# Performance work log

Hardware: AMD Instinct MI355X
Metric: run time of the kernel (lower is better)

Reference implementation:

```python
import jax, jax.numpy as jnp
import numpy as np

# Constants derived from init_kwargs / input shapes
B = 4          # number of graphs (equal-sized point clouds)
N = 16384      # points per graph
STRIDE = 4     # center_sampler: strided sampling, ratio 0.25 -> M = N/4
K = 20         # k nearest neighbors
N_SCAL = 16    # reps '16x0+16x1': 16 scalars
N_VEC = 16     # 16 vectors (3 coeffs each)
D = N_SCAL + 3 * N_VEC   # 64 feature coeffs
HID = 128
OUT = 128


def transform_coeffs(x, R):
    """TensorReps('16x0+16x1') coefficient transform: scalars unchanged,
    each 3-vector v -> R @ v.  x: [n, D], R: [n, 3, 3]."""
    s = x[:, :N_SCAL]
    v = x[:, N_SCAL:].reshape(-1, N_VEC, 3)
    v = jnp.einsum('nab,nkb->nka', R, v)
    return jnp.concatenate([s, v.reshape(-1, 3 * N_VEC)], axis=-1)


def setup_inputs() -> dict:
    key = jax.random.key(0)
    ks = jax.random.split(key, 6)
    Ntot = B * N
    x = jax.random.normal(ks[0], (Ntot, D), jnp.float32)
    pos = jax.random.normal(ks[1], (Ntot, 3), jnp.float32)
    # orthonormal local frames via QR of random 3x3 matrices
    lf = jax.random.normal(ks[2], (Ntot, 3, 3), jnp.float32)
    lframes, _ = jnp.linalg.qr(lf)
    batch = jnp.repeat(jnp.arange(B, dtype=jnp.int32), N)
    W1 = jax.random.normal(ks[3], (2 * D, HID), jnp.float32) / np.sqrt(2 * D)
    b1 = jnp.zeros((HID,), jnp.float32)
    W2 = jax.random.normal(ks[4], (HID, OUT), jnp.float32) / np.sqrt(HID)
    b2 = jnp.zeros((OUT,), jnp.float32)
    return {"x": x, "pos": pos, "lframes": lframes, "batch": batch,
            "W1": W1, "b1": b1, "W2": W2, "b2": b2}


def reference(x, pos, lframes, batch, W1, b1, W2, b2):
    M = N // STRIDE
    # --- center_sampler: strided sampling per graph (CustomPointSampler) ---
    idx = (jnp.arange(B)[:, None] * N + jnp.arange(0, N, STRIDE)[None, :]).reshape(-1)  # [B*M]

    # --- transform features to global frame: coeffs with lframes^T ---
    kf = transform_coeffs(x, jnp.swapaxes(lframes, -1, -2))
    # --- concat_pos_to_features (transform_pos=False) ---
    kf = jnp.concatenate([kf, pos], axis=-1)            # [Ntot, 67]
    Dk = kf.shape[-1]

    # --- brute-force per-graph kNN: centers query against all nodes ---
    kf_b = kf.reshape(B, N, Dk)
    q = kf_b[:, ::STRIDE]                               # [B, M, Dk] centers
    d2 = (jnp.sum(q * q, -1)[:, :, None]
          + jnp.sum(kf_b * kf_b, -1)[:, None, :]
          - 2.0 * jnp.einsum('bmd,bnd->bmn', q, kf_b))  # [B, M, N]
    _, nbr = jax.lax.top_k(-d2, K)                      # [B, M, K] per-graph idx
    src = nbr + (jnp.arange(B) * N)[:, None, None]      # global node idx

    # --- gather dst/src node data ---
    x_dst = x[idx].reshape(B, M, D)
    lf_dst = lframes[idx]                               # [B*M, 3, 3]
    x_src = x[src.reshape(-1)].reshape(B, M, K, D)

    # --- EdgeConv (tensor-frames flavor): relative features rotated into the
    #     destination local frame, MLP over [x_i, R_i (x_j - x_i)], max-aggr ---
    rel = x_src - x_dst[:, :, None]                     # [B, M, K, D]
    R_edge = jnp.repeat(lf_dst, K, axis=0)              # [B*M*K, 3, 3]
    rel_local = transform_coeffs(rel.reshape(-1, D), R_edge).reshape(B, M, K, D)
    h = jnp.concatenate(
        [jnp.broadcast_to(x_dst[:, :, None], rel.shape), rel_local], axis=-1)  # [B,M,K,2D]
    msg = jax.nn.relu(h @ W1 + b1) @ W2 + b2            # [B, M, K, OUT]
    out = jnp.max(msg, axis=2).reshape(B * M, OUT)

    return out, pos[idx], batch[idx], lf_dst
```

## Files before the change

kernel.cpp:

```cpp
#include <hip/hip_runtime.h>
#include <hip/hip_bf16.h>

#define NTOT 65536
#define KNN  20
#define KROW 104

typedef __attribute__((ext_vector_type(4))) float f32x4;
typedef __attribute__((ext_vector_type(8))) short s16x8;

#define WS_NORM 13631488
#define WS_NBR  13893632
#define WS_WT1  15204352
#define WS_WT2  15237120
#define WS_MG   15269888

#define ROWS 144
#define CSTR 257
#define OFF_TAUG 149056
#define KNN_SMEM 149312
#define THRESH 64

__device__ __forceinline__ unsigned short f2bf_rne(float v){
  unsigned u = __float_as_uint(v);
  return (unsigned short)((u + 0x7FFFu + ((u >> 16) & 1u)) >> 16);
}

__global__ __launch_bounds__(256) void k_prep(const float* __restrict__ x,
        const float* __restrict__ pos, const float* __restrict__ lfr,
        unsigned short* __restrict__ kfB, float* __restrict__ normB){
  int n = blockIdx.x * 256 + threadIdx.x;
  const float* xr = x + n * 64;
  float R[9];
  #pragma unroll
  for (int j = 0; j < 9; j++) R[j] = lfr[n * 9 + j];
  float c[67];
  #pragma unroll
  for (int i = 0; i < 16; i++) c[i] = xr[i];
  #pragma unroll
  for (int k = 0; k < 16; k++){
    float v0 = xr[16 + 3*k], v1 = xr[17 + 3*k], v2 = xr[18 + 3*k];
    #pragma unroll
    for (int a = 0; a < 3; a++)
      c[16 + 3*k + a] = R[a] * v0 + R[3 + a] * v1 + R[6 + a] * v2;
  }
  #pragma unroll
  for (int a = 0; a < 3; a++) c[64 + a] = pos[n * 3 + a];
  float sq = 0.f;
  #pragma unroll
  for (int d = 0; d < 67; d++) sq += c[d] * c[d];
  __attribute__((aligned(16))) unsigned short row[KROW];
  #pragma unroll
  for (int d = 0; d < 67; d++) row[d] = f2bf_rne(c[d]);
  #pragma unroll
  for (int d = 67; d < KROW; d++) row[d] = 0;
  uint4* dst = (uint4*)(kfB + (size_t)n * KROW);
  const uint4* s4 = (const uint4*)row;
  #pragma unroll
  for (int i = 0; i < 13; i++) dst[i] = s4[i];
  normB[n] = sq;
}

__global__ __launch_bounds__(256) void k_wprep(const float* __restrict__ W1,
        const float* __restrict__ W2, unsigned short* __restrict__ wb1,
        unsigned short* __restrict__ wb2){
  int a = blockIdx.x * 256 + threadIdx.x;
  int kb = a >> 12, n = (a >> 5) & 127, kl = a & 31;
  int i = ((kb << 5) + kl) * 128 + n;
  wb1[a] = f2bf_rne(W1[i]);
  wb2[a] = f2bf_rne(W2[i]);
}

__device__ __forceinline__ unsigned col_compact(unsigned* buf,
    int col, int cn, int lane){
  unsigned e0 = (lane < cn) ? buf[lane * CSTR + col] : 0xFFFFFFFFu;
  unsigned e1 = (lane + 64 < cn) ? buf[(lane + 64) * CSTR + col] : 0xFFFFFFFFu;
  unsigned T = 0;
  #pragma unroll 1
  for (int b = 31; b >= 0; --b){
    unsigned cand = T | (1u << b);
    int c = __popcll(__ballot(e0 < cand)) + __popcll(__ballot(e1 < cand));
    if (c <= 31) T = cand;
  }
  unsigned long long m0 = __ballot(e0 <= T);
  unsigned long long m1 = __ballot(e1 <= T);
  int b1 = __popcll(m0);
  unsigned long long ltm = (1ull << lane) - 1ull;
  if (e0 <= T) buf[__popcll(m0 & ltm) * CSTR + col] = e0;
  if (e1 <= T) buf[(b1 + __popcll(m1 & ltm)) * CSTR + col] = e1;
  return T;
}

__global__ __launch_bounds__(1024, 4) void k_knn(
    const unsigned short* __restrict__ kfB, const float* __restrict__ normB,
    unsigned short* __restrict__ mgG){
  __shared__ __attribute__((aligned(16))) char smem[KNN_SMEM];
  unsigned* buf = (unsigned*)smem;
  unsigned* tauG = (unsigned*)(smem + OFF_TAUG);

  int tid = threadIdx.x;
  int blk = blockIdx.x;
  int b = blk & 3;
  int qloc0 = (blk >> 2) << 6;
  int bbase = b << 14;

  if (tid < 64) tauG[tid] = 0x7F7FC000u;

  int lane = tid & 63;
  int wv = tid >> 6;
  int wq = wv >> 2;
  int kq = wv & 3;
  int l15 = lane & 15, quad = lane >> 4;
  int colB = (wq << 6) + kq;

  int qloc = qloc0 + (wq << 4);
  s16x8 af[3];
  {
    int nodeA = bbase + ((qloc + l15) << 2);
    const unsigned short* ap = kfB + (size_t)nodeA * KROW + quad * 8;
    af[0] = *(const s16x8*)(ap);
    af[1] = *(const s16x8*)(ap + 32);
    af[2] = *(const s16x8*)(ap + 64);
  }
  float qsq[4];
  #pragma unroll
  for (int r = 0; r < 4; r++)
    qsq[r] = normB[bbase + ((qloc + (quad << 2) + r) << 2)];

  float tauR[4] = {3.0e38f, 3.0e38f, 3.0e38f, 3.0e38f};
  int cntR[4];

  const unsigned short* kp = kfB + (size_t)(bbase + (kq << 12) + l15) * KROW + quad * 8;
  const float* np = normB + (bbase + (kq << 12) + l15);

  __syncthreads();

  s16x8 cK[4][3];
  float nK[4];
  #define LOADK(S) do { \
      cK[S][0] = *(const s16x8*)(kp); \
      cK[S][1] = *(const s16x8*)(kp + 32); \
      cK[S][2] = *(const s16x8*)(kp + 64); \
      nK[S] = *np; kp += 16 * KROW; np += 16; } while (0)

  auto comp = [&](const s16x8 bf[3], float ksqv, float d2v[4]){
    f32x4 acc = (f32x4){0.f, 0.f, 0.f, 0.f};
    acc = __builtin_amdgcn_mfma_f32_16x16x32_bf16(af[0], bf[0], acc, 0, 0, 0);
    acc = __builtin_amdgcn_mfma_f32_16x16x32_bf16(af[1], bf[1], acc, 0, 0, 0);
    acc = __builtin_amdgcn_mfma_f32_16x16x32_bf16(af[2], bf[2], acc, 0, 0, 0);
    #pragma unroll
    for (int r = 0; r < 4; r++)
      d2v[r] = fmaxf(qsq[r] + ksqv - 2.f * acc[r], 0.f);
  };

  auto seed = [&](const float d2v[4], int g){
    int kidx = (kq << 12) + (g << 4) + l15;
    #pragma unroll
    for (int r = 0; r < 4; r++){
      unsigned pk = ((__float_as_uint(d2v[r]) + 0x2000u) & 0xFFFFC000u) | (unsigned)kidx;
      buf[((g << 4) + l15) * CSTR + colB + (quad << 4) + (r << 2)] = pk;
    }
  };

  auto process = [&](const float d2v[4], int g){
    bool p[4];
    #pragma unroll
    for (int r = 0; r < 4; r++) p[r] = d2v[r] < tauR[r];
    if (__any(p[0] | p[1] | p[2] | p[3])){
      int kidx = (kq << 12) + (g << 4) + l15;
      #pragma unroll
      for (int r = 0; r < 4; r++){
        unsigned long long m = __ballot(p[r]);
        if (m){
          int lo = (int)((m >> (quad << 4)) & 0xFFFFull);
          if (lo){
            int colr = colB + (quad << 4) + (r << 2);
            int pre = __popc(lo & ((1 << l15) - 1));
            if (p[r]){
              unsigned pk = ((__float_as_uint(d2v[r]) + 0x2000u) & 0xFFFFC000u) | (unsigned)kidx;
              buf[(cntR[r] + pre) * CSTR + colr] = pk;
            }
            cntR[r] += __popc(lo);
          }
        }
      }
    }
  };

  auto check_compact = [&](int limit){
    #pragma unroll
    for (int r = 0; r < 4; r++){
      unsigned long long mr = __ballot(cntR[r] > limit);
      while (mr){
        int ldr = __ffsll((unsigned long long)mr) - 1;
        int qd = ldr >> 4;
        mr &= ~(0xFFFFull << (qd << 4));
        int col = colB + (qd << 4) + (r << 2);
        int cn = __shfl(cntR[r], qd << 4, 64);
        unsigned T = col_compact(buf, col, cn, lane);
        if (quad == qd) cntR[r] = 32;
        if (lane == 0) atomicMin(&tauG[(wq << 4) + (qd << 2) + r], T);
      }
    }
  };

  float d2v[4];
  LOADK(0); LOADK(1); LOADK(2); LOADK(3);
  #pragma unroll
  for (int j = 0; j < 4; j++){
    comp(cK[j], nK[j], d2v);
    seed(d2v, j);
    LOADK(j);
  }
  #pragma unroll
  for (int r = 0; r < 4; r++) cntR[r] = 64;

  #pragma unroll 1
  for (int g = 4; g < 256; g += 4){
    #pragma unroll
    for (int j = 0; j < 4; j++){
      comp(cK[j], nK[j], d2v);
      LOADK(j);
      process(d2v, g + j);
    }
    check_compact(THRESH);
    uint4 tg = *(const uint4*)&tauG[(wq << 4) + (quad << 2)];
    tauR[0] = __uint_as_float(tg.x & 0xFFFFC000u);
    tauR[1] = __uint_as_float(tg.y & 0xFFFFC000u);
    tauR[2] = __uint_as_float(tg.z & 0xFFFFC000u);
    tauR[3] = __uint_as_float(tg.w & 0xFFFFC000u);
  }

  check_compact(32);
  __syncthreads();

  #pragma unroll 1
  for (int s = 0; s < 4; s++){
    int q = (wv << 2) + s;
    int qid = (b << 12) + qloc0 + q;
    unsigned e0 = buf[(lane & 31) * CSTR + (q << 2) + (lane >> 5)];
    unsigned e1 = buf[(lane & 31) * CSTR + (q << 2) + 2 + (lane >> 5)];
    unsigned T = 0;
    #pragma unroll 1
    for (int bb = 31; bb >= 0; --bb){
      unsigned cand = T | (1u << bb);
      int c = __popcll(__ballot(e0 < cand)) + __popcll(__ballot(e1 < cand));
      if (c <= 31) T = cand;
    }
    unsigned long long m0 = __ballot(e0 <= T);
    unsigned long long m1 = __ballot(e1 <= T);
    int b1 = __popcll(m0);
    unsigned long long ltm = (1ull << lane) - 1ull;
    int p0 = __popcll(m0 & ltm);
    int p1 = b1 + __popcll(m1 & ltm);
    if ((e0 <= T) && (p0 < 32)) mgG[qid * 32 + p0] = (unsigned short)(e0 & 0x3FFFu);
    if ((e1 <= T) && (p1 < 32)) mgG[qid * 32 + p1] = (unsigned short)(e1 & 0x3FFFu);
  }
}

__global__ __launch_bounds__(256) void k_rerank(const float* __restrict__ x,
    const float* __restrict__ pos, const float* __restrict__ lfr,
    const unsigned short* __restrict__ mgG, int* __restrict__ nbr){
  __shared__ double qkf[8][68];
  int tid = threadIdx.x;
  int ql = tid >> 5;
  int j  = tid & 31;
  int qid = blockIdx.x * 8 + ql;
  int b = qid >> 12;
  int bbase = b << 14;
  int node_q = bbase + ((qid & 4095) << 2);

  {
    const float* xr = x + node_q * 64;
    for (int dd = j; dd < 67; dd += 32){
      double val;
      if (dd < 16) val = (double)xr[dd];
      else if (dd < 64){
        int r = dd - 16; int k = r / 3; int a = r - 3 * k;
        val = (double)lfr[node_q*9 + a]     * (double)xr[16 + 3*k]
            + (double)lfr[node_q*9 + 3 + a] * (double)xr[17 + 3*k]
            + (double)lfr[node_q*9 + 6 + a] * (double)xr[18 + 3*k];
      } else val = (double)pos[node_q*3 + (dd - 64)];
      qkf[ql][dd] = val;
    }
  }
  __syncthreads();

  int idx = (int)mgG[qid * 32 + j];
  int node = bbase + idx;
  const float* xr = x + node * 64;
  double R[9];
  #pragma unroll
  for (int t = 0; t < 9; t++) R[t] = (double)lfr[node * 9 + t];
  double d2 = 0.0;
  #pragma unroll
  for (int dd = 0; dd < 16; dd++){ double t = (double)xr[dd] - qkf[ql][dd]; d2 += t * t; }
  #pragma unroll
  for (int k = 0; k < 16; k++){
    double v0 = xr[16 + 3*k], v1 = xr[17 + 3*k], v2 = xr[18 + 3*k];
    #pragma unroll
    for (int a = 0; a < 3; a++){
      double val = R[a] * v0 + R[3 + a] * v1 + R[6 + a] * v2;
      double t = val - qkf[ql][16 + 3*k + a]; d2 += t * t;
    }
  }
  #pragma unroll
  for (int a = 0; a < 3; a++){ double t = (double)pos[node*3 + a] - qkf[ql][64 + a]; d2 += t * t; }

  int base = (tid & 32) ? 32 : 0;
  int rank = 0;
  #pragma unroll 1
  for (int j2 = 0; j2 < 32; j2++){
    double o = __shfl(d2, base + j2, 64);
    rank += (o < d2) || ((o == d2) && (j2 < j));
  }
  if (rank < KNN) nbr[qid * KNN + rank] = node;
}

#define M_X   0
#define M_H   43520
#define M_W1  84480
#define M_W2  117248
#define M_B1  150016
#define M_B2  150528
#define M_NBR 151040
#define M_XD  151680
#define M_LF  153728
#define M_SZ  154048

__global__ __launch_bounds__(512) void k_mlp(const float* __restrict__ x,
    const float* __restrict__ lfr, const int* __restrict__ nbr,
    const unsigned short* __restrict__ wb1, const unsigned short* __restrict__ wb2,
    const float* __restrict__ b1, const float* __restrict__ b2,
    float* __restrict__ out){
  __shared__ __attribute__((aligned(16))) char smem[M_SZ];
  float* xsF = (float*)(smem + M_X);
  unsigned short* a1B = (unsigned short*)(smem + M_X);
  unsigned short* hB = (unsigned short*)(smem + M_H);
  unsigned short* wt1 = (unsigned short*)(smem + M_W1);
  unsigned short* wt2 = (unsigned short*)(smem + M_W2);
  float* b1L = (float*)(smem + M_B1);
  float* b2L = (float*)(smem + M_B2);
  int*   nbrL = (int*)(smem + M_NBR);
  float* xdL  = (float*)(smem + M_XD);
  float* lfL  = (float*)(smem + M_LF);

  int tid = threadIdx.x;
  int qid0 = blockIdx.x * 8;
  int lane = tid & 63, wv = tid >> 6;
  int l15 = lane & 15, quad = lane >> 4;

  {
    const uint4* g1 = (const uint4*)wb1;
    const uint4* g2 = (const uint4*)wb2;
    uint4* l1 = (uint4*)wt1;
    uint4* l2 = (uint4*)wt2;
    #pragma unroll
    for (int p = 0; p < 4; p++){
      l1[tid + (p << 9)] = g1[tid + (p << 9)];
      l2[tid + (p << 9)] = g2[tid + (p << 9)];
    }
  }
  if (tid < 160) nbrL[tid] = nbr[qid0 * 20 + tid];
  {
    int q = tid >> 6, d = tid & 63;
    int qid = qid0 + q;
    int node = ((qid >> 12) << 14) + ((qid & 4095) << 2);
    xdL[q * 64 + d] = x[node * 64 + d];
  }
  if (tid < 72){
    int q = tid / 9, j = tid - 9 * q;
    int qid = qid0 + q;
    int node = ((qid >> 12) << 14) + ((qid & 4095) << 2);
    lfL[q * 9 + j] = lfr[node * 9 + j];
  }
  if (tid < 128){ b1L[tid] = b1[tid]; b2L[tid] = b2[tid]; }
  __syncthreads();

  {
    int f4 = tid & 15;
    #pragma unroll
    for (int p = 0; p < 5; p++){
      int e = (tid >> 4) + (p << 5);
      float4 v = *(const float4*)&x[(size_t)nbrL[e] * 64 + (f4 << 2)];
      *(float4*)&xsF[e * 68 + (f4 << 2)] = v;
    }
  }
  __syncthreads();

  {
    int d = tid & 127, eo = tid >> 7;
    int cls, kk = 0, aa = 0;
    if (d < 64) cls = 0;
    else { int dd = d - 64;
      if (dd < 16) cls = 1;
      else { cls = 2; int r = dd - 16; kk = (r * 21846) >> 16; aa = r - 3 * kk; } }
    int hoff = ((d >> 5) * 160) * 32 + (d & 31);
    #pragma unroll 4
    for (int p = 0; p < 40; p++){
      int e = eo + (p << 2);
      int q = (e * 3277) >> 16;
      float v;
      if (cls == 0) v = xdL[q * 64 + d];
      else if (cls == 1) v = xsF[e * 68 + (d - 64)] - xdL[q * 64 + (d - 64)];
      else {
        int base = 16 + 3 * kk;
        float u0 = xsF[e * 68 + base]     - xdL[q * 64 + base];
        float u1 = xsF[e * 68 + base + 1] - xdL[q * 64 + base + 1];
        float u2 = xsF[e * 68 + base + 2] - xdL[q * 64 + base + 2];
        v = lfL[q * 9 + aa * 3] * u0 + lfL[q * 9 + aa * 3 + 1] * u1 + lfL[q * 9 + aa * 3 + 2] * u2;
      }
      hB[hoff + e * 32] = f2bf_rne(v);
    }
  }
  __syncthreads();

  {
    s16x8 bfr[4];
    #pragma unroll
    for (int ks = 0; ks < 4; ks++)
      bfr[ks] = *(const s16x8*)(wt1 + ((ks * 128 + (wv << 4) + l15) * 32 + (quad << 3)));
    float b1v = b1L[(wv << 4) + l15];
    int colhi = wv >> 1, collo = ((wv & 1) << 4) + l15;
    #pragma unroll
    for (int mt = 0; mt < 10; mt++){
      f32x4 acc = (f32x4){0.f, 0.f, 0.f, 0.f};
      #pragma unroll
      for (int ks = 0; ks < 4; ks++){
        s16x8 af = *(const s16x8*)(hB + ((ks * 160 + (mt << 4) + l15) * 32 + (quad << 3)));
        acc = __builtin_amdgcn_mfma_f32_16x16x32_bf16(af, bfr[ks], acc, 0, 0, 0);
      }
      #pragma unroll
      for (int r = 0; r < 4; r++){
        float v = fmaxf(acc[r] + b1v, 0.f);
        int row = (mt << 4) + (quad << 2) + r;
        a1B[(colhi * 160 + row) * 32 + collo] = f2bf_rne(v);
      }
    }
  }
  __syncthreads();

  {
    s16x8 bfr[4];
    #pragma unroll
    for (int ks = 0; ks < 4; ks++)
      bfr[ks] = *(const s16x8*)(wt2 + ((ks * 128 + (wv << 4) + l15) * 32 + (quad << 3)));
    float mxv[8];
    #pragma unroll
    for (int q = 0; q < 8; q++) mxv[q] = -3.0e38f;
    const int QA[10]  = {0,0,1,2,3,4,4,5,6,7};
    const int CUT[10] = {16,4,8,12,16,16,4,8,12,16};
    #pragma unroll
    for (int mt = 0; mt < 10; mt++){
      f32x4 acc = (f32x4){0.f, 0.f, 0.f, 0.f};
      #pragma unroll
      for (int ks = 0; ks < 4; ks++){
        s16x8 af = *(const s16x8*)(a1B + ((ks * 160 + (mt << 4) + l15) * 32 + (quad << 3)));
        acc = __builtin_amdgcn_mfma_f32_16x16x32_bf16(af, bfr[ks], acc, 0, 0, 0);
      }
      int qa = QA[mt], cut = CUT[mt];
      if (cut >= 16){
        #pragma unroll
        for (int r = 0; r < 4; r++) mxv[qa] = fmaxf(mxv[qa], acc[r]);
      } else {
        #pragma unroll
        for (int r = 0; r < 4; r++){
          int lr = (quad << 2) + r;
          bool toA = lr < cut;
          mxv[qa]     = fmaxf(mxv[qa],     toA ? acc[r] : -3.0e38f);
          mxv[qa + 1] = fmaxf(mxv[qa + 1], toA ? -3.0e38f : acc[r]);
        }
      }
    }
    #pragma unroll
    for (int q = 0; q < 8; q++){
      float v = mxv[q];
      v = fmaxf(v, __shfl_xor(v, 16, 64));
      v = fmaxf(v, __shfl_xor(v, 32, 64));
      mxv[q] = v;
    }
    if (quad == 0){
      int col = (wv << 4) + l15;
      float b2v = b2L[col];
      #pragma unroll
      for (int q = 0; q < 8; q++)
        out[(size_t)(qid0 + q) * 128 + col] = mxv[q] + b2v;
    }
  }
}

__global__ __launch_bounds__(256) void k_tail(const float* __restrict__ pos,
    const float* __restrict__ lfr, float* __restrict__ out){
  int q = blockIdx.x * 256 + threadIdx.x;
  int b = q >> 12;
  int node = (b << 14) + ((q & 4095) << 2);
  float* o_pos = out + 2097152;
  float* o_bat = out + 2146304;
  float* o_lf  = out + 2162688;
  #pragma unroll
  for (int j = 0; j < 3; j++) o_pos[q * 3 + j] = pos[node * 3 + j];
  o_bat[q] = (float)b;
  #pragma unroll
  for (int j = 0; j < 9; j++) o_lf[q * 9 + j] = lfr[node * 9 + j];
}

extern "C" void kernel_launch(void* const* d_in, const int* in_sizes, int n_in,
                              void* d_out, int out_size, void* d_ws, size_t ws_size,
                              hipStream_t stream){
  const float* x   = (const float*)d_in[0];
  const float* pos = (const float*)d_in[1];
  const float* lfr = (const float*)d_in[2];
  const float* W1  = (const float*)d_in[4];
  const float* b1  = (const float*)d_in[5];
  const float* W2  = (const float*)d_in[6];
  const float* b2  = (const float*)d_in[7];

  unsigned short* kfB = (unsigned short*)d_ws;
  float* normB = (float*)((char*)d_ws + WS_NORM);
  int*   nbr   = (int*)((char*)d_ws + WS_NBR);
  unsigned short* wb1 = (unsigned short*)((char*)d_ws + WS_WT1);
  unsigned short* wb2 = (unsigned short*)((char*)d_ws + WS_WT2);
  unsigned short* mgG = (unsigned short*)((char*)d_ws + WS_MG);
  float* out = (float*)d_out;

  hipLaunchKernelGGL(k_prep,   dim3(256),  dim3(256),  0, stream, x, pos, lfr, kfB, normB);
  hipLaunchKernelGGL(k_wprep,  dim3(64),   dim3(256),  0, stream, W1, W2, wb1, wb2);
  hipLaunchKernelGGL(k_knn,    dim3(256),  dim3(1024), 0, stream, kfB, normB, mgG);
  hipLaunchKernelGGL(k_rerank, dim3(2048), dim3(256),  0, stream, x, pos, lfr, mgG, nbr);
  hipLaunchKernelGGL(k_mlp,    dim3(2048), dim3(512),  0, stream, x, lfr, nbr, wb1, wb2, b1, b2, out);
  hipLaunchKernelGGL(k_tail,   dim3(64),   dim3(256),  0, stream, pos, lfr, out);
}
```

Measured before the change: 597.4 us.

## Coarsen kNN compaction threshold bits and load MLP weights directly to registers

The in-loop candidate compaction now searches only the upper 18 bits of the key, keeping every candidate at or below the coarse threshold and returning that count, which cuts ballot iterations per compaction. The exact 32-entry compaction runs only in the final pass. The MLP kernel no longer stages W1/W2 in shared memory; each wave loads its weight fragments straight from global memory into registers, shrinking LDS use so more blocks can be resident per CU. The risks are more candidates kept after each coarse compaction, which can trigger compactions more often, and extra register pressure from the weight fragments.

Result: faster. 535.6 us (-10.3%).

```diff
diff --git a/kernel.cpp b/kernel.cpp
--- a/kernel.cpp
+++ b/kernel.cpp
@@ -70,7 +70,7 @@
   wb2[a] = f2bf_rne(W2[i]);
 }
 
-__device__ __forceinline__ unsigned col_compact(unsigned* buf,
+__device__ __forceinline__ unsigned col_compact32(unsigned* buf,
     int col, int cn, int lane){
   unsigned e0 = (lane < cn) ? buf[lane * CSTR + col] : 0xFFFFFFFFu;
   unsigned e1 = (lane + 64 < cn) ? buf[(lane + 64) * CSTR + col] : 0xFFFFFFFFu;
@@ -88,6 +88,28 @@
   if (e0 <= T) buf[__popcll(m0 & ltm) * CSTR + col] = e0;
   if (e1 <= T) buf[(b1 + __popcll(m1 & ltm)) * CSTR + col] = e1;
   return T;
+}
+
+__device__ __forceinline__ unsigned col_compact18(unsigned* buf,
+    int col, int cn, int lane){
+  unsigned e0 = (lane < cn) ? buf[lane * CSTR + col] : 0xFFFFFFFFu;
+  unsigned e1 = (lane + 64 < cn) ? buf[(lane + 64) * CSTR + col] : 0xFFFFFFFFu;
+  unsigned T = 0;
+  #pragma unroll 1
+  for (int b = 31; b >= 14; --b){
+    unsigned cand = T | (1u << b);
+    int c = __popcll(__ballot(e0 < cand)) + __popcll(__ballot(e1 < cand));
+    if (c <= 31) T = cand;
+  }
+  unsigned th = T >> 14;
+  unsigned long long m0 = __ballot((e0 >> 14) <= th);
+  unsigned long long m1 = __ballot((e1 >> 14) <= th);
+  int b1 = __popcll(m0);
+  int kc = b1 + __popcll(m1);
+  unsigned long long ltm = (1ull << lane) - 1ull;
+  if ((e0 >> 14) <= th) buf[__popcll(m0 & ltm) * CSTR + col] = e0;
+  if ((e1 >> 14) <= th) buf[(b1 + __popcll(m1 & ltm)) * CSTR + col] = e1;
+  return T | (unsigned)kc;
 }
 
 __global__ __launch_bounds__(1024, 4) void k_knn(
@@ -196,9 +218,9 @@
         mr &= ~(0xFFFFull << (qd << 4));
         int col = colB + (qd << 4) + (r << 2);
         int cn = __shfl(cntR[r], qd << 4, 64);
-        unsigned T = col_compact(buf, col, cn, lane);
-        if (quad == qd) cntR[r] = 32;
-        if (lane == 0) atomicMin(&tauG[(wq << 4) + (qd << 2) + r], T);
+        unsigned Tk = col_compact18(buf, col, cn, lane);
+        if (quad == qd) cntR[r] = (int)(Tk & 0x3FFFu);
+        if (lane == 0) atomicMin(&tauG[(wq << 4) + (qd << 2) + r], Tk & 0xFFFFC000u);
       }
     }
   };
@@ -230,7 +252,21 @@
     tauR[3] = __uint_as_float(tg.w & 0xFFFFC000u);
   }
 
-  check_compact(32);
+  {
+    #pragma unroll
+    for (int r = 0; r < 4; r++){
+      unsigned long long mr = __ballot(cntR[r] > 32);
+      while (mr){
+        int ldr = __ffsll((unsigned long long)mr) - 1;
+        int qd = ldr >> 4;
+        mr &= ~(0xFFFFull << (qd << 4));
+        int col = colB + (qd << 4) + (r << 2);
+        int cn = __shfl(cntR[r], qd << 4, 64);
+        col_compact32(buf, col, cn, lane);
+        if (quad == qd) cntR[r] = 32;
+      }
+    }
+  }
   __syncthreads();
 
   #pragma unroll 1
@@ -318,14 +354,12 @@
 
 #define M_X   0
 #define M_H   43520
-#define M_W1  84480
-#define M_W2  117248
-#define M_B1  150016
-#define M_B2  150528
-#define M_NBR 151040
-#define M_XD  151680
-#define M_LF  153728
-#define M_SZ  154048
+#define M_B1  84480
+#define M_B2  84992
+#define M_NBR 85504
+#define M_XD  86144
+#define M_LF  88192
+#define M_SZ  88512
 
 __global__ __launch_bounds__(512) void k_mlp(const float* __restrict__ x,
     const float* __restrict__ lfr, const int* __restrict__ nbr,
@@ -336,8 +370,6 @@
   float* xsF = (float*)(smem + M_X);
   unsigned short* a1B = (unsigned short*)(smem + M_X);
   unsigned short* hB = (unsigned short*)(smem + M_H);
-  unsigned short* wt1 = (unsigned short*)(smem + M_W1);
-  unsigned short* wt2 = (unsigned short*)(smem + M_W2);
   float* b1L = (float*)(smem + M_B1);
   float* b2L = (float*)(smem + M_B2);
   int*   nbrL = (int*)(smem + M_NBR);
@@ -349,17 +381,14 @@
   int lane = tid & 63, wv = tid >> 6;
   int l15 = lane & 15, quad = lane >> 4;
 
-  {
-    const uint4* g1 = (const uint4*)wb1;
-    const uint4* g2 = (const uint4*)wb2;
-    uint4* l1 = (uint4*)wt1;
-    uint4* l2 = (uint4*)wt2;
-    #pragma unroll
-    for (int p = 0; p < 4; p++){
-      l1[tid + (p << 9)] = g1[tid + (p << 9)];
-      l2[tid + (p << 9)] = g2[tid + (p << 9)];
-    }
-  }
+  s16x8 wf1[4], wf2[4];
+  #pragma unroll
+  for (int ks = 0; ks < 4; ks++){
+    int a = (ks * 128 + (wv << 4) + l15) * 32 + (quad << 3);
+    wf1[ks] = *(const s16x8*)(wb1 + a);
+    wf2[ks] = *(const s16x8*)(wb2 + a);
+  }
+
   if (tid < 160) nbrL[tid] = nbr[qid0 * 20 + tid];
   {
     int q = tid >> 6, d = tid & 63;
@@ -415,10 +444,6 @@
   __syncthreads();
 
   {
-    s16x8 bfr[4];
-    #pragma unroll
-    for (int ks = 0; ks < 4; ks++)
-      bfr[ks] = *(const s16x8*)(wt1 + ((ks * 128 + (wv << 4) + l15) * 32 + (quad << 3)));
     float b1v = b1L[(wv << 4) + l15];
     int colhi = wv >> 1, collo = ((wv & 1) << 4) + l15;
     #pragma unroll
@@ -427,7 +452,7 @@
       #pragma unroll
       for (int ks = 0; ks < 4; ks++){
         s16x8 af = *(const s16x8*)(hB + ((ks * 160 + (mt << 4) + l15) * 32 + (quad << 3)));
-        acc = __builtin_amdgcn_mfma_f32_16x16x32_bf16(af, bfr[ks], acc, 0, 0, 0);
+        acc = __builtin_amdgcn_mfma_f32_16x16x32_bf16(af, wf1[ks], acc, 0, 0, 0);
       }
       #pragma unroll
       for (int r = 0; r < 4; r++){
@@ -440,10 +465,6 @@
   __syncthreads();
 
   {
-    s16x8 bfr[4];
-    #pragma unroll
-    for (int ks = 0; ks < 4; ks++)
-      bfr[ks] = *(const s16x8*)(wt2 + ((ks * 128 + (wv << 4) + l15) * 32 + (quad << 3)));
     float mxv[8];
     #pragma unroll
     for (int q = 0; q < 8; q++) mxv[q] = -3.0e38f;
@@ -455,7 +476,7 @@
       #pragma unroll
       for (int ks = 0; ks < 4; ks++){
         s16x8 af = *(const s16x8*)(a1B + ((ks * 160 + (mt << 4) + l15) * 32 + (quad << 3)));
-        acc = __builtin_amdgcn_mfma_f32_16x16x32_bf16(af, bfr[ks], acc, 0, 0, 0);
+        acc = __builtin_amdgcn_mfma_f32_16x16x32_bf16(af, wf2[ks], acc, 0, 0, 0);
       }
       int qa = QA[mt], cut = CUT[mt];
       if (cut >= 16){
```
